# Performance work log

Hardware: AMD Instinct MI355X
Metric: run time of the kernel (lower is better)

The kernel has to match this reference:

```python
import jax, jax.numpy as jnp
import numpy as np

D = 1024       # hidden_size
H = 16         # num_heads
DH = D // H    # d_keys = d_values = 64
FF = int(D * 2.0)  # mlp hidden
EPS = 1e-6


def _ln(t):
    # LayerNorm, elementwise_affine=False
    mu = jnp.mean(t, axis=-1, keepdims=True)
    var = jnp.mean((t - mu) ** 2, axis=-1, keepdims=True)
    return (t - mu) * jax.lax.rsqrt(var + EPS)


def setup_inputs() -> dict:
    key = jax.random.key(0)
    ks = jax.random.split(key, 16)
    B, L = 2, 2048
    s = 0.02
    return {
        "x": jax.random.normal(ks[0], (B, L, D), jnp.float32),
        "c": jax.random.normal(ks[1], (B, 1, D), jnp.float32),
        "Wq": jax.random.normal(ks[2], (D, D), jnp.float32) * s,
        "bq": jnp.zeros((D,), jnp.float32),
        "Wk": jax.random.normal(ks[3], (D, D), jnp.float32) * s,
        "bk": jnp.zeros((D,), jnp.float32),
        "Wv": jax.random.normal(ks[4], (D, D), jnp.float32) * s,
        "bv": jnp.zeros((D,), jnp.float32),
        "Wo": jax.random.normal(ks[5], (D, D), jnp.float32) * s,
        "bo": jnp.zeros((D,), jnp.float32),
        "W1": jax.random.normal(ks[6], (D, FF), jnp.float32) * s,
        "b1": jnp.zeros((FF,), jnp.float32),
        "W2": jax.random.normal(ks[7], (FF, D), jnp.float32) * s,
        "b2": jnp.zeros((D,), jnp.float32),
        "Wada": jax.random.normal(ks[8], (D, 6 * D), jnp.float32) * s,
        "bada": jnp.zeros((6 * D,), jnp.float32),
    }


def reference(x, c, Wq, bq, Wk, bk, Wv, bv, Wo, bo, W1, b1, W2, b2, Wada, bada):
    B, L, _ = x.shape
    # adaLN-Zero modulation params (dropout layers act as identity in eval)
    ada = jax.nn.silu(c) @ Wada + bada  # [B,1,6D]
    shift_msa, scale_msa, gate_msa, shift_mlp, scale_mlp, gate_mlp = jnp.split(ada, 6, axis=-1)

    # --- attention branch ---
    h = _ln(x) * (1.0 + scale_msa) + shift_msa
    q = (h @ Wq + bq).reshape(B, L, H, DH)
    k = (h @ Wk + bk).reshape(B, L, H, DH)
    v = (h @ Wv + bv).reshape(B, L, H, DH)
    scale = 1.0 / np.sqrt(DH).astype(np.float32)
    scores = jnp.einsum('blhe,bshe->bhls', q, k)  # full LxL scores, as in source
    A = jax.nn.softmax(scale * scores, axis=-1)
    out = jnp.einsum('bhls,bshd->blhd', A, v)     # [B,L,H,DH]
    # mix=True: transpose(2,1) then view(B,L,-1) -> head/position mixing reshape
    out = jnp.transpose(out, (0, 2, 1, 3)).reshape(B, L, H * DH)
    x = x + gate_msa * (out @ Wo + bo)

    # --- MLP branch (exact GELU: nn.GELU() passed as act_layer) ---
    h2 = _ln(x) * (1.0 + scale_mlp) + shift_mlp
    m = jax.nn.gelu(h2 @ W1 + b1, approximate=False) @ W2 + b2
    return x + gate_mlp * m
```

## Files before the change

kernel.cpp:

```cpp
#include <hip/hip_runtime.h>
#include <hip/hip_bf16.h>

typedef unsigned short ushort_t;
typedef __bf16 bf16x8 __attribute__((ext_vector_type(8)));
typedef float f32x4 __attribute__((ext_vector_type(4)));

typedef unsigned int u32;
typedef u32 __attribute__((address_space(1))) global_u32;
typedef u32 __attribute__((address_space(3))) lds_u32;

#define D_ 1024
#define L_ 2048
#define B_ 2
#define H_ 16
#define DH_ 64
#define FF_ 2048
#define ADA_ 6144
#define BHL_ (B_ * H_ * L_)
#define PSTR 136

#define MFMA __builtin_amdgcn_mfma_f32_16x16x32_bf16

__device__ __forceinline__ ushort_t f2bf(float f) {
    union { float f; u32 u; } v; v.f = f;
    u32 r = v.u + 0x7fffu + ((v.u >> 16) & 1u);
    return (ushort_t)(r >> 16);
}

__device__ __forceinline__ void llds16(const ushort_t* src, ushort_t* dst) {
    __builtin_amdgcn_global_load_lds((global_u32*)src, (lds_u32*)dst, 16, 0, 0);
}

__global__ void transpose_w(const float* __restrict__ W, ushort_t* __restrict__ Wt,
                            int K, int N) {
    __shared__ float tile[64][65];
    int n0 = blockIdx.x * 64, k0 = blockIdx.y * 64;
    int t = threadIdx.x;
    for (int p = 0; p < 4; ++p) {
        int k = p * 16 + (t >> 4), nn = (t & 15) * 4;
        float4 v = *(const float4*)(W + (size_t)(k0 + k) * N + n0 + nn);
        tile[k][nn] = v.x; tile[k][nn + 1] = v.y; tile[k][nn + 2] = v.z; tile[k][nn + 3] = v.w;
    }
    __syncthreads();
    for (int p = 0; p < 4; ++p) {
        int n = p * 16 + (t >> 4), kk = (t & 15) * 4;
        ushort4 o;
        o.x = f2bf(tile[kk][n]); o.y = f2bf(tile[kk + 1][n]);
        o.z = f2bf(tile[kk + 2][n]); o.w = f2bf(tile[kk + 3][n]);
        *(ushort4*)(Wt + (size_t)(n0 + n) * K + k0 + kk) = o;
    }
}

__global__ void transpose_v(const ushort_t* __restrict__ V, ushort_t* __restrict__ Vt) {
    __shared__ ushort_t tile[64][72];
    int bh = blockIdx.y, l0 = blockIdx.x * 64;
    const ushort_t* Vb = V + ((size_t)bh * L_ + l0) * DH_;
    ushort_t* Vtb = Vt + (size_t)bh * DH_ * L_;
    int t = threadIdx.x;
    for (int p = 0; p < 2; ++p) {
        int i = p * 32 + (t >> 3), d0 = (t & 7) * 8;
        ushort4 v0 = *(const ushort4*)(Vb + (size_t)i * DH_ + d0);
        ushort4 v1 = *(const ushort4*)(Vb + (size_t)i * DH_ + d0 + 4);
        tile[d0 + 0][i] = v0.x; tile[d0 + 1][i] = v0.y; tile[d0 + 2][i] = v0.z; tile[d0 + 3][i] = v0.w;
        tile[d0 + 4][i] = v1.x; tile[d0 + 5][i] = v1.y; tile[d0 + 6][i] = v1.z; tile[d0 + 7][i] = v1.w;
    }
    __syncthreads();
    for (int p = 0; p < 2; ++p) {
        int dh = p * 32 + (t >> 3), j0 = (t & 7) * 8;
        ushort4 o0, o1;
        o0.x = tile[dh][j0 + 0]; o0.y = tile[dh][j0 + 1]; o0.z = tile[dh][j0 + 2]; o0.w = tile[dh][j0 + 3];
        o1.x = tile[dh][j0 + 4]; o1.y = tile[dh][j0 + 5]; o1.z = tile[dh][j0 + 6]; o1.w = tile[dh][j0 + 7];
        *(ushort4*)(Vtb + (size_t)dh * L_ + l0 + j0) = o0;
        *(ushort4*)(Vtb + (size_t)dh * L_ + l0 + j0 + 4) = o1;
    }
}

__global__ void ada_gemv(const float* __restrict__ c, const float* __restrict__ Wada,
                         float* __restrict__ partial) {
    int ks = blockIdx.y;
    int j = blockIdx.x * 256 + threadIdx.x;
    __shared__ float s0[64], s1[64];
    if (threadIdx.x < 64) {
        float v = c[ks * 64 + threadIdx.x];
        s0[threadIdx.x] = v / (1.f + __expf(-v));
        v = c[D_ + ks * 64 + threadIdx.x];
        s1[threadIdx.x] = v / (1.f + __expf(-v));
    }
    __syncthreads();
    float a0 = 0.f, a1 = 0.f;
#pragma unroll 8
    for (int d = 0; d < 64; ++d) {
        float w = Wada[(size_t)(ks * 64 + d) * ADA_ + j];
        a0 = fmaf(s0[d], w, a0);
        a1 = fmaf(s1[d], w, a1);
    }
    partial[(size_t)(ks * 2 + 0) * ADA_ + j] = a0;
    partial[(size_t)(ks * 2 + 1) * ADA_ + j] = a1;
}

__global__ void ada_reduce(const float* __restrict__ partial,
                           const float* __restrict__ bada, float* __restrict__ ada) {
    int j = blockIdx.x * 256 + threadIdx.x;
    float a0 = bada[j], a1 = bada[j];
#pragma unroll
    for (int ks = 0; ks < 16; ++ks) {
        a0 += partial[(size_t)(ks * 2 + 0) * ADA_ + j];
        a1 += partial[(size_t)(ks * 2 + 1) * ADA_ + j];
    }
    ada[j] = a0;
    ada[ADA_ + j] = a1;
}

__global__ void ln_mod(const float* __restrict__ x, const float* __restrict__ ada,
                       int so, int co, ushort_t* __restrict__ out) {
    int row = blockIdx.x;
    int b = row >> 11;
    float4 v = ((const float4*)(x + (size_t)row * D_))[threadIdx.x];
    float sum = v.x + v.y + v.z + v.w;
    float sq = v.x * v.x + v.y * v.y + v.z * v.z + v.w * v.w;
    for (int off = 32; off; off >>= 1) { sum += __shfl_down(sum, off); sq += __shfl_down(sq, off); }
    __shared__ float sa[4], sb[4];
    int wave = threadIdx.x >> 6, lane = threadIdx.x & 63;
    if (lane == 0) { sa[wave] = sum; sb[wave] = sq; }
    __syncthreads();
    sum = sa[0] + sa[1] + sa[2] + sa[3];
    sq = sb[0] + sb[1] + sb[2] + sb[3];
    float mean = sum * (1.f / 1024.f);
    float var = sq * (1.f / 1024.f) - mean * mean;
    float rstd = rsqrtf(var + 1e-6f);
    int d = threadIdx.x * 4;
    const float* shf = ada + (size_t)b * ADA_ + so;
    const float* scf = ada + (size_t)b * ADA_ + co;
    ushort4 ov;
    ov.x = f2bf((v.x - mean) * rstd * (1.f + scf[d + 0]) + shf[d + 0]);
    ov.y = f2bf((v.y - mean) * rstd * (1.f + scf[d + 1]) + shf[d + 1]);
    ov.z = f2bf((v.z - mean) * rstd * (1.f + scf[d + 2]) + shf[d + 2]);
    ov.w = f2bf((v.w - mean) * rstd * (1.f + scf[d + 3]) + shf[d + 3]);
    *(ushort4*)(out + (size_t)row * D_ + d) = ov;
}

struct EpiArgs {
    const float* bias0; const float* bias1; const float* bias2;
    ushort_t* o0; ushort_t* o1; ushort_t* o2;
    const float* resid; const float* gate;
    float* fout;
};

template <int EPI>
__device__ __forceinline__ void epi_store(float v, int m, int n, int N, const EpiArgs& e) {
    if (EPI == 0) {
        int which = n >> 10, cc = n & 1023;
        const float* bias = which == 0 ? e.bias0 : which == 1 ? e.bias1 : e.bias2;
        ushort_t* ob = which == 0 ? e.o0 : which == 1 ? e.o1 : e.o2;
        v += bias[cc];
        if (which == 0) v *= 0.18033688f;
        int b = m >> 11, l = m & 2047, h = cc >> 6, dh = cc & 63;
        ob[(((size_t)(b * H_ + h) * L_) + l) * DH_ + dh] = f2bf(v);
    } else if (EPI == 1) {
        v += e.bias0[n];
        v = 0.5f * v * (1.f + erff(v * 0.70710678118f));
        e.o0[(size_t)m * N + n] = f2bf(v);
    } else {
        int b = m >> 11;
        e.fout[(size_t)m * N + n] =
            e.resid[(size_t)m * N + n] + e.gate[(size_t)b * ADA_ + n] * (v + e.bias0[n]);
    }
}

template <int EPI>
__device__ __forceinline__ void st4(const f32x4& cc, int mb, int n, int N, const EpiArgs& e) {
#pragma unroll
    for (int r = 0; r < 4; ++r) epi_store<EPI>(cc[r], mb + r, n, N, e);
}

template <int EPI>
__global__ __launch_bounds__(256, 2) void gemm_bt(
    const ushort_t* __restrict__ A, const ushort_t* __restrict__ Bt,
    int M, int N, int K, EpiArgs e) {
    __shared__ ushort_t As[128 * 64];
    __shared__ ushort_t Bs[128 * 64];
    int m0 = blockIdx.x * 128, n0 = blockIdx.y * 128;
    int tid = threadIdx.x, wave = tid >> 6, lane = tid & 63;
    int quad = lane >> 4, lc = lane & 15;
    int wm = (wave & 1) * 64, wn = (wave >> 1) * 64;
    int srow = lane >> 3, sg = lane & 7;
    int sw = lc & 7;

    f32x4 c00 = {}, c01 = {}, c02 = {}, c03 = {};
    f32x4 c10 = {}, c11 = {}, c12 = {}, c13 = {};
    f32x4 c20 = {}, c21 = {}, c22 = {}, c23 = {};
    f32x4 c30 = {}, c31 = {}, c32 = {}, c33 = {};

    for (int k0 = 0; k0 < K; k0 += 64) {
#pragma unroll
        for (int i = 0; i < 8; ++i) {
            int chunk = wave * 8 + i;
            int c = chunk & 15;
            int row = c * 8 + srow;
            int g = sg ^ (row & 7);
            if (chunk < 16)
                llds16(A + (size_t)(m0 + row) * K + k0 + g * 8, &As[c * 512 + lane * 8]);
            else
                llds16(Bt + (size_t)(n0 + row) * K + k0 + g * 8, &Bs[c * 512 + lane * 8]);
        }
        __syncthreads();
#pragma unroll
        for (int kk = 0; kk < 2; ++kk) {
            int off = ((kk * 4 + quad) ^ sw) * 8;
            bf16x8 a0 = *(const bf16x8*)&As[(wm +  0 + lc) * 64 + off];
            bf16x8 a1 = *(const bf16x8*)&As[(wm + 16 + lc) * 64 + off];
            bf16x8 a2 = *(const bf16x8*)&As[(wm + 32 + lc) * 64 + off];
            bf16x8 a3 = *(const bf16x8*)&As[(wm + 48 + lc) * 64 + off];
            bf16x8 b0 = *(const bf16x8*)&Bs[(wn +  0 + lc) * 64 + off];
            bf16x8 b1 = *(const bf16x8*)&Bs[(wn + 16 + lc) * 64 + off];
            bf16x8 b2 = *(const bf16x8*)&Bs[(wn + 32 + lc) * 64 + off];
            bf16x8 b3 = *(const bf16x8*)&Bs[(wn + 48 + lc) * 64 + off];
            c00 = MFMA(a0, b0, c00, 0, 0, 0); c01 = MFMA(a0, b1, c01, 0, 0, 0);
            c02 = MFMA(a0, b2, c02, 0, 0, 0); c03 = MFMA(a0, b3, c03, 0, 0, 0);
            c10 = MFMA(a1, b0, c10, 0, 0, 0); c11 = MFMA(a1, b1, c11, 0, 0, 0);
            c12 = MFMA(a1, b2, c12, 0, 0, 0); c13 = MFMA(a1, b3, c13, 0, 0, 0);
            c20 = MFMA(a2, b0, c20, 0, 0, 0); c21 = MFMA(a2, b1, c21, 0, 0, 0);
            c22 = MFMA(a2, b2, c22, 0, 0, 0); c23 = MFMA(a2, b3, c23, 0, 0, 0);
            c30 = MFMA(a3, b0, c30, 0, 0, 0); c31 = MFMA(a3, b1, c31, 0, 0, 0);
            c32 = MFMA(a3, b2, c32, 0, 0, 0); c33 = MFMA(a3, b3, c33, 0, 0, 0);
        }
        __syncthreads();
    }

    int mb = m0 + wm + quad * 4, nb = n0 + wn + lc;
    st4<EPI>(c00, mb +  0, nb +  0, N, e); st4<EPI>(c01, mb +  0, nb + 16, N, e);
    st4<EPI>(c02, mb +  0, nb + 32, N, e); st4<EPI>(c03, mb +  0, nb + 48, N, e);
    st4<EPI>(c10, mb + 16, nb +  0, N, e); st4<EPI>(c11, mb + 16, nb + 16, N, e);
    st4<EPI>(c12, mb + 16, nb + 32, N, e); st4<EPI>(c13, mb + 16, nb + 48, N, e);
    st4<EPI>(c20, mb + 32, nb +  0, N, e); st4<EPI>(c21, mb + 32, nb + 16, N, e);
    st4<EPI>(c22, mb + 32, nb + 32, N, e); st4<EPI>(c23, mb + 32, nb + 48, N, e);
    st4<EPI>(c30, mb + 48, nb +  0, N, e); st4<EPI>(c31, mb + 48, nb + 16, N, e);
    st4<EPI>(c32, mb + 48, nb + 32, N, e); st4<EPI>(c33, mb + 48, nb + 48, N, e);
}

__global__ __launch_bounds__(256, 2) void attn(
    const ushort_t* __restrict__ Q, const ushort_t* __restrict__ Kx,
    const ushort_t* __restrict__ Vt,
    ushort_t* __restrict__ Op0, ushort_t* __restrict__ Op1,
    float* __restrict__ lsum) {
    __shared__ ushort_t Ks[128 * 64];
    __shared__ ushort_t Vs[64 * 128];
    __shared__ ushort_t Ps[4 * 16 * PSTR];
    int id = blockIdx.x;
    int bh = ((id & 7) << 2) + ((id >> 3) & 3);
    int half = (id >> 5) & 1;
    int qt = id >> 6;
    const ushort_t* Qg = Q + ((size_t)bh * L_ + qt * 128) * DH_;
    const ushort_t* Kg = Kx + (size_t)bh * L_ * DH_;
    const ushort_t* Vg = Vt + (size_t)bh * DH_ * L_;
    int tid = threadIdx.x, wave = tid >> 6, lane = tid & 63;
    int quad = lane >> 4, lc = lane & 15;
    int sw = lc & 7;
    int srow = lane >> 3, sg = lane & 7;

    const ushort_t* qp = Qg + (size_t)(wave * 32 + lc) * DH_ + quad * 8;
    bf16x8 q00 = *(const bf16x8*)(qp);
    bf16x8 q01 = *(const bf16x8*)(qp + 32);
    bf16x8 q10 = *(const bf16x8*)(qp + 16 * DH_);
    bf16x8 q11 = *(const bf16x8*)(qp + 16 * DH_ + 32);

    f32x4 o00 = {}, o01 = {}, o02 = {}, o03 = {};
    f32x4 o10 = {}, o11 = {}, o12 = {}, o13 = {};
    float lrow0 = 0.f, lrow1 = 0.f;
    ushort_t* Pw = &Ps[wave * 16 * PSTR];

    for (int t = half * 8; t < half * 8 + 8; ++t) {
#pragma unroll
        for (int i = 0; i < 8; ++i) {
            int chunk = wave * 8 + i;
            if (chunk < 16) {
                int row = chunk * 8 + srow;
                int g = sg ^ (row & 7);
                llds16(Kg + ((size_t)(t * 128 + row)) * DH_ + g * 8, &Ks[chunk * 512 + lane * 8]);
            } else {
                int c2 = chunk - 16;
                int row = c2 * 4 + (lane >> 4);
                int g = (lane & 15) ^ (row & 15);
                llds16(Vg + (size_t)row * L_ + t * 128 + g * 8, &Vs[c2 * 512 + lane * 8]);
            }
        }
        __syncthreads();

        f32x4 s[2][8];
#pragma unroll
        for (int kk = 0; kk < 2; ++kk) {
            int off = ((kk * 4 + quad) ^ sw) * 8;
            bf16x8 aq0 = kk == 0 ? q00 : q01;
            bf16x8 aq1 = kk == 0 ? q10 : q11;
#pragma unroll
            for (int ni = 0; ni < 8; ++ni) {
                bf16x8 bk = *(const bf16x8*)&Ks[(ni * 16 + lc) * 64 + off];
                if (kk == 0) {
                    f32x4 z = {0.f, 0.f, 0.f, 0.f};
                    s[0][ni] = MFMA(bk, aq0, z, 0, 0, 0);
                    s[1][ni] = MFMA(bk, aq1, z, 0, 0, 0);
                } else {
                    s[0][ni] = MFMA(bk, aq0, s[0][ni], 0, 0, 0);
                    s[1][ni] = MFMA(bk, aq1, s[1][ni], 0, 0, 0);
                }
            }
        }

#pragma unroll
        for (int pi = 0; pi < 2; ++pi) {
            float acc = 0.f;
#pragma unroll
            for (int ni = 0; ni < 8; ++ni) {
                float p0 = __builtin_amdgcn_exp2f(s[pi][ni][0]);
                float p1 = __builtin_amdgcn_exp2f(s[pi][ni][1]);
                float p2 = __builtin_amdgcn_exp2f(s[pi][ni][2]);
                float p3 = __builtin_amdgcn_exp2f(s[pi][ni][3]);
                acc += (p0 + p1) + (p2 + p3);
                u32 lo = (u32)f2bf(p0) | ((u32)f2bf(p1) << 16);
                u32 hi = (u32)f2bf(p2) | ((u32)f2bf(p3) << 16);
                uint2 pk; pk.x = lo; pk.y = hi;
                *(uint2*)&Pw[lc * PSTR + ni * 16 + quad * 4] = pk;
            }
            acc += __shfl_xor(acc, 16);
            acc += __shfl_xor(acc, 32);
            if (pi == 0) lrow0 += acc; else lrow1 += acc;

#pragma unroll
            for (int kk = 0; kk < 4; ++kk) {
                int gq = kk * 4 + quad;
                bf16x8 ap  = *(const bf16x8*)&Pw[lc * PSTR + gq * 8];
                bf16x8 bv0 = *(const bf16x8*)&Vs[( 0 + lc) * 128 + ((gq ^ lc) * 8)];
                bf16x8 bv1 = *(const bf16x8*)&Vs[(16 + lc) * 128 + ((gq ^ lc) * 8)];
                bf16x8 bv2 = *(const bf16x8*)&Vs[(32 + lc) * 128 + ((gq ^ lc) * 8)];
                bf16x8 bv3 = *(const bf16x8*)&Vs[(48 + lc) * 128 + ((gq ^ lc) * 8)];
                if (pi == 0) {
                    o00 = MFMA(ap, bv0, o00, 0, 0, 0); o01 = MFMA(ap, bv1, o01, 0, 0, 0);
                    o02 = MFMA(ap, bv2, o02, 0, 0, 0); o03 = MFMA(ap, bv3, o03, 0, 0, 0);
                } else {
                    o10 = MFMA(ap, bv0, o10, 0, 0, 0); o11 = MFMA(ap, bv1, o11, 0, 0, 0);
                    o12 = MFMA(ap, bv2, o12, 0, 0, 0); o13 = MFMA(ap, bv3, o13, 0, 0, 0);
                }
            }
        }
        __syncthreads();
    }

    ushort_t* Op = half ? Op1 : Op0;
#pragma unroll
    for (int pi = 0; pi < 2; ++pi) {
#pragma unroll
        for (int nio = 0; nio < 4; ++nio) {
            const f32x4& ov = pi == 0 ? (nio == 0 ? o00 : nio == 1 ? o01 : nio == 2 ? o02 : o03)
                                      : (nio == 0 ? o10 : nio == 1 ? o11 : nio == 2 ? o12 : o13);
#pragma unroll
            for (int r = 0; r < 4; ++r) {
                int row = qt * 128 + wave * 32 + pi * 16 + quad * 4 + r;
                Op[((size_t)bh * L_ + row) * DH_ + nio * 16 + lc] = f2bf(ov[r]);
            }
        }
    }
    if (quad == 0) {
        int base = qt * 128 + wave * 32;
        lsum[(size_t)half * BHL_ + (size_t)bh * L_ + base + lc] = lrow0;
        lsum[(size_t)half * BHL_ + (size_t)bh * L_ + base + 16 + lc] = lrow1;
    }
}

__global__ void attn_merge(const ushort_t* __restrict__ Op0,
                           const ushort_t* __restrict__ Op1,
                           const float* __restrict__ lsum,
                           ushort_t* __restrict__ O) {
    int gid = blockIdx.x * 256 + threadIdx.x;
    int row = gid >> 3, j = gid & 7;
    float inv = 1.f / (lsum[row] + lsum[BHL_ + row]);
    bf16x8 v0 = *(const bf16x8*)(Op0 + (size_t)row * DH_ + j * 8);
    bf16x8 v1 = *(const bf16x8*)(Op1 + (size_t)row * DH_ + j * 8);
    ushort4 lo, hi;
    lo.x = f2bf(((float)v0[0] + (float)v1[0]) * inv);
    lo.y = f2bf(((float)v0[1] + (float)v1[1]) * inv);
    lo.z = f2bf(((float)v0[2] + (float)v1[2]) * inv);
    lo.w = f2bf(((float)v0[3] + (float)v1[3]) * inv);
    hi.x = f2bf(((float)v0[4] + (float)v1[4]) * inv);
    hi.y = f2bf(((float)v0[5] + (float)v1[5]) * inv);
    hi.z = f2bf(((float)v0[6] + (float)v1[6]) * inv);
    hi.w = f2bf(((float)v0[7] + (float)v1[7]) * inv);
    *(ushort4*)(O + (size_t)row * DH_ + j * 8) = lo;
    *(ushort4*)(O + (size_t)row * DH_ + j * 8 + 4) = hi;
}

extern "C" void kernel_launch(void* const* d_in, const int* in_sizes, int n_in,
                              void* d_out, int out_size, void* d_ws, size_t ws_size,
                              hipStream_t stream) {
    (void)in_sizes; (void)n_in; (void)out_size; (void)ws_size;
    const float* x    = (const float*)d_in[0];
    const float* c    = (const float*)d_in[1];
    const float* Wq   = (const float*)d_in[2];
    const float* bq   = (const float*)d_in[3];
    const float* Wk   = (const float*)d_in[4];
    const float* bk   = (const float*)d_in[5];
    const float* Wv   = (const float*)d_in[6];
    const float* bv   = (const float*)d_in[7];
    const float* Wo   = (const float*)d_in[8];
    const float* bo   = (const float*)d_in[9];
    const float* W1   = (const float*)d_in[10];
    const float* b1   = (const float*)d_in[11];
    const float* W2   = (const float*)d_in[12];
    const float* b2   = (const float*)d_in[13];
    const float* Wada = (const float*)d_in[14];
    const float* bada = (const float*)d_in[15];

    char* w = (char*)d_ws;
    float*    ada  = (float*)(w + 0);
    ushort_t* Wqkv = (ushort_t*)(w + 49152);
    ushort_t* Wo_t = (ushort_t*)(w + 6340608);
    ushort_t* W1_t = (ushort_t*)(w + 8437760);
    ushort_t* W2_t = (ushort_t*)(w + 12632064);
    ushort_t* h    = (ushort_t*)(w + 16826368);
    ushort_t* Qb   = (ushort_t*)(w + 25214976);
    ushort_t* Kb   = (ushort_t*)(w + 33603584);
    ushort_t* Vb   = (ushort_t*)(w + 41992192);
    ushort_t* Vtb  = (ushort_t*)(w + 50380800);
    float*    x1   = (float*)(w + 58769408);
    ushort_t* Ob   = Qb;
    ushort_t* m1   = Qb;
    float*    lsb  = x1;
    float*    adap = (float*)Vtb;

    const int M = B_ * L_;

    transpose_w<<<dim3(16, 16), 256, 0, stream>>>(Wq, Wqkv + 0,             D_, D_);
    transpose_w<<<dim3(16, 16), 256, 0, stream>>>(Wk, Wqkv + 1024 * 1024,   D_, D_);
    transpose_w<<<dim3(16, 16), 256, 0, stream>>>(Wv, Wqkv + 2 * 1024 * 1024, D_, D_);
    transpose_w<<<dim3(16, 16), 256, 0, stream>>>(Wo, Wo_t, D_, D_);
    transpose_w<<<dim3(32, 16), 256, 0, stream>>>(W1, W1_t, D_, FF_);
    transpose_w<<<dim3(16, 32), 256, 0, stream>>>(W2, W2_t, FF_, D_);

    ada_gemv<<<dim3(24, 16), 256, 0, stream>>>(c, Wada, adap);
    ada_reduce<<<24, 256, 0, stream>>>(adap, bada, ada);
    ln_mod<<<M, 256, 0, stream>>>(x, ada, 0, 1024, h);

    EpiArgs e0 = {bq, bk, bv, Qb, Kb, Vb, nullptr, nullptr, nullptr};
    gemm_bt<0><<<dim3(32, 24), 256, 0, stream>>>(h, Wqkv, M, 3072, D_, e0);

    transpose_v<<<dim3(32, 32), 256, 0, stream>>>(Vb, Vtb);

    attn<<<1024, 256, 0, stream>>>(Qb, Kb, Vtb, Vb, h, lsb);
    attn_merge<<<2048, 256, 0, stream>>>(Vb, h, lsb, Ob);

    EpiArgs e1 = {bo, nullptr, nullptr, nullptr, nullptr, nullptr, x, ada + 2048, x1};
    gemm_bt<2><<<dim3(32, 8), 256, 0, stream>>>(Ob, Wo_t, M, D_, D_, e1);

    ln_mod<<<M, 256, 0, stream>>>(x1, ada, 3072, 4096, h);

    EpiArgs e2 = {b1, nullptr, nullptr, m1, nullptr, nullptr, nullptr, nullptr, nullptr};
    gemm_bt<1><<<dim3(32, 16), 256, 0, stream>>>(h, W1_t, M, FF_, D_, e2);

    EpiArgs e3 = {b2, nullptr, nullptr, nullptr, nullptr, nullptr, x1, ada + 5120, (float*)d_out};
    gemm_bt<2><<<dim3(32, 8), 256, 0, stream>>>(m1, W2_t, M, D_, FF_, e3);
}
```

Measured before the change: 370.8 us.

## Merge weight transposes, add 64-row GEMM for small grids, swizzle P tile

Folds the six weight-transpose launches into one 2048-block kernel to cut launch overhead. Adds a gemm_bt64 variant with 64x128 tiles and uses it for the Wo, W1 and W2 GEMMs, doubling the block count so the grid fills more of the GPU's compute units (a 256-block grid is smaller than the device). Replaces the padded P buffer in attention with an XOR-swizzled 128-wide layout to save LDS while avoiding bank conflicts. The smaller tiles lower per-block data reuse and raise total global and LDS traffic.

Measured after the change: 341.2 us. 1.09x faster.

```diff
diff --git a/kernel.cpp b/kernel.cpp
--- a/kernel.cpp
+++ b/kernel.cpp
@@ -17,7 +17,6 @@
 #define FF_ 2048
 #define ADA_ 6144
 #define BHL_ (B_ * H_ * L_)
-#define PSTR 136
 
 #define MFMA __builtin_amdgcn_mfma_f32_16x16x32_bf16
 
@@ -31,10 +30,25 @@
     __builtin_amdgcn_global_load_lds((global_u32*)src, (lds_u32*)dst, 16, 0, 0);
 }
 
-__global__ void transpose_w(const float* __restrict__ W, ushort_t* __restrict__ Wt,
-                            int K, int N) {
+__global__ void transpose_w_all(
+    const float* __restrict__ Wq, const float* __restrict__ Wk,
+    const float* __restrict__ Wv, const float* __restrict__ Wo,
+    const float* __restrict__ W1, const float* __restrict__ W2,
+    ushort_t* __restrict__ Wqkv, ushort_t* __restrict__ Wo_t,
+    ushort_t* __restrict__ W1_t, ushort_t* __restrict__ W2_t) {
     __shared__ float tile[64][65];
-    int n0 = blockIdx.x * 64, k0 = blockIdx.y * 64;
+    int id = blockIdx.x;
+    const float* W; ushort_t* Wt; int K, N, ntx, lid;
+    if (id < 1024) {
+        int which = id >> 8; lid = id & 255; K = 1024; N = 1024; ntx = 16;
+        W  = which == 0 ? Wq : which == 1 ? Wk : which == 2 ? Wv : Wo;
+        Wt = which == 3 ? Wo_t : Wqkv + (size_t)which * 1024 * 1024;
+    } else if (id < 1536) {
+        lid = id - 1024; W = W1; Wt = W1_t; K = 1024; N = 2048; ntx = 32;
+    } else {
+        lid = id - 1536; W = W2; Wt = W2_t; K = 2048; N = 1024; ntx = 16;
+    }
+    int n0 = (lid % ntx) * 64, k0 = (lid / ntx) * 64;
     int t = threadIdx.x;
     for (int p = 0; p < 4; ++p) {
         int k = p * 16 + (t >> 4), nn = (t & 15) * 4;
@@ -238,6 +252,64 @@
     st4<EPI>(c32, mb + 48, nb + 32, N, e); st4<EPI>(c33, mb + 48, nb + 48, N, e);
 }
 
+template <int EPI>
+__global__ __launch_bounds__(256, 2) void gemm_bt64(
+    const ushort_t* __restrict__ A, const ushort_t* __restrict__ Bt,
+    int M, int N, int K, EpiArgs e) {
+    __shared__ ushort_t As[64 * 64];
+    __shared__ ushort_t Bs[128 * 64];
+    int m0 = blockIdx.x * 64, n0 = blockIdx.y * 128;
+    int tid = threadIdx.x, wave = tid >> 6, lane = tid & 63;
+    int quad = lane >> 4, lc = lane & 15;
+    int wn = wave * 32;
+    int srow = lane >> 3, sg = lane & 7;
+    int sw = lc & 7;
+
+    f32x4 c00 = {}, c01 = {};
+    f32x4 c10 = {}, c11 = {};
+    f32x4 c20 = {}, c21 = {};
+    f32x4 c30 = {}, c31 = {};
+
+    for (int k0 = 0; k0 < K; k0 += 64) {
+#pragma unroll
+        for (int i = 0; i < 6; ++i) {
+            int chunk = wave * 6 + i;
+            if (chunk < 8) {
+                int row = chunk * 8 + srow;
+                int g = sg ^ (row & 7);
+                llds16(A + (size_t)(m0 + row) * K + k0 + g * 8, &As[chunk * 512 + lane * 8]);
+            } else {
+                int c = chunk - 8;
+                int row = c * 8 + srow;
+                int g = sg ^ (row & 7);
+                llds16(Bt + (size_t)(n0 + row) * K + k0 + g * 8, &Bs[c * 512 + lane * 8]);
+            }
+        }
+        __syncthreads();
+#pragma unroll
+        for (int kk = 0; kk < 2; ++kk) {
+            int off = ((kk * 4 + quad) ^ sw) * 8;
+            bf16x8 a0 = *(const bf16x8*)&As[( 0 + lc) * 64 + off];
+            bf16x8 a1 = *(const bf16x8*)&As[(16 + lc) * 64 + off];
+            bf16x8 a2 = *(const bf16x8*)&As[(32 + lc) * 64 + off];
+            bf16x8 a3 = *(const bf16x8*)&As[(48 + lc) * 64 + off];
+            bf16x8 b0 = *(const bf16x8*)&Bs[(wn +  0 + lc) * 64 + off];
+            bf16x8 b1 = *(const bf16x8*)&Bs[(wn + 16 + lc) * 64 + off];
+            c00 = MFMA(a0, b0, c00, 0, 0, 0); c01 = MFMA(a0, b1, c01, 0, 0, 0);
+            c10 = MFMA(a1, b0, c10, 0, 0, 0); c11 = MFMA(a1, b1, c11, 0, 0, 0);
+            c20 = MFMA(a2, b0, c20, 0, 0, 0); c21 = MFMA(a2, b1, c21, 0, 0, 0);
+            c30 = MFMA(a3, b0, c30, 0, 0, 0); c31 = MFMA(a3, b1, c31, 0, 0, 0);
+        }
+        __syncthreads();
+    }
+
+    int mb = m0 + quad * 4, nb = n0 + wn + lc;
+    st4<EPI>(c00, mb +  0, nb + 0, N, e); st4<EPI>(c01, mb +  0, nb + 16, N, e);
+    st4<EPI>(c10, mb + 16, nb + 0, N, e); st4<EPI>(c11, mb + 16, nb + 16, N, e);
+    st4<EPI>(c20, mb + 32, nb + 0, N, e); st4<EPI>(c21, mb + 32, nb + 16, N, e);
+    st4<EPI>(c30, mb + 48, nb + 0, N, e); st4<EPI>(c31, mb + 48, nb + 16, N, e);
+}
+
 __global__ __launch_bounds__(256, 2) void attn(
     const ushort_t* __restrict__ Q, const ushort_t* __restrict__ Kx,
     const ushort_t* __restrict__ Vt,
@@ -245,7 +317,7 @@
     float* __restrict__ lsum) {
     __shared__ ushort_t Ks[128 * 64];
     __shared__ ushort_t Vs[64 * 128];
-    __shared__ ushort_t Ps[4 * 16 * PSTR];
+    __shared__ ushort_t Ps[4 * 16 * 128];
     int id = blockIdx.x;
     int bh = ((id & 7) << 2) + ((id >> 3) & 3);
     int half = (id >> 5) & 1;
@@ -267,7 +339,7 @@
     f32x4 o00 = {}, o01 = {}, o02 = {}, o03 = {};
     f32x4 o10 = {}, o11 = {}, o12 = {}, o13 = {};
     float lrow0 = 0.f, lrow1 = 0.f;
-    ushort_t* Pw = &Ps[wave * 16 * PSTR];
+    ushort_t* Pw = &Ps[wave * 16 * 128];
 
     for (int t = half * 8; t < half * 8 + 8; ++t) {
 #pragma unroll
@@ -319,7 +391,8 @@
                 u32 lo = (u32)f2bf(p0) | ((u32)f2bf(p1) << 16);
                 u32 hi = (u32)f2bf(p2) | ((u32)f2bf(p3) << 16);
                 uint2 pk; pk.x = lo; pk.y = hi;
-                *(uint2*)&Pw[lc * PSTR + ni * 16 + quad * 4] = pk;
+                int cg = ni * 2 + (quad >> 1);
+                *(uint2*)&Pw[lc * 128 + ((cg ^ lc) & 15) * 8 + (quad & 1) * 4] = pk;
             }
             acc += __shfl_xor(acc, 16);
             acc += __shfl_xor(acc, 32);
@@ -328,7 +401,7 @@
 #pragma unroll
             for (int kk = 0; kk < 4; ++kk) {
                 int gq = kk * 4 + quad;
-                bf16x8 ap  = *(const bf16x8*)&Pw[lc * PSTR + gq * 8];
+                bf16x8 ap  = *(const bf16x8*)&Pw[lc * 128 + ((gq ^ lc) & 15) * 8];
                 bf16x8 bv0 = *(const bf16x8*)&Vs[( 0 + lc) * 128 + ((gq ^ lc) * 8)];
                 bf16x8 bv1 = *(const bf16x8*)&Vs[(16 + lc) * 128 + ((gq ^ lc) * 8)];
                 bf16x8 bv2 = *(const bf16x8*)&Vs[(32 + lc) * 128 + ((gq ^ lc) * 8)];
@@ -428,12 +501,8 @@
 
     const int M = B_ * L_;
 
-    transpose_w<<<dim3(16, 16), 256, 0, stream>>>(Wq, Wqkv + 0,             D_, D_);
-    transpose_w<<<dim3(16, 16), 256, 0, stream>>>(Wk, Wqkv + 1024 * 1024,   D_, D_);
-    transpose_w<<<dim3(16, 16), 256, 0, stream>>>(Wv, Wqkv + 2 * 1024 * 1024, D_, D_);
-    transpose_w<<<dim3(16, 16), 256, 0, stream>>>(Wo, Wo_t, D_, D_);
-    transpose_w<<<dim3(32, 16), 256, 0, stream>>>(W1, W1_t, D_, FF_);
-    transpose_w<<<dim3(16, 32), 256, 0, stream>>>(W2, W2_t, FF_, D_);
+    transpose_w_all<<<2048, 256, 0, stream>>>(Wq, Wk, Wv, Wo, W1, W2,
+                                              Wqkv, Wo_t, W1_t, W2_t);
 
     ada_gemv<<<dim3(24, 16), 256, 0, stream>>>(c, Wada, adap);
     ada_reduce<<<24, 256, 0, stream>>>(adap, bada, ada);
@@ -448,13 +517,13 @@
     attn_merge<<<2048, 256, 0, stream>>>(Vb, h, lsb, Ob);
 
     EpiArgs e1 = {bo, nullptr, nullptr, nullptr, nullptr, nullptr, x, ada + 2048, x1};
-    gemm_bt<2><<<dim3(32, 8), 256, 0, stream>>>(Ob, Wo_t, M, D_, D_, e1);
+    gemm_bt64<2><<<dim3(64, 8), 256, 0, stream>>>(Ob, Wo_t, M, D_, D_, e1);
 
     ln_mod<<<M, 256, 0, stream>>>(x1, ada, 3072, 4096, h);
 
     EpiArgs e2 = {b1, nullptr, nullptr, m1, nullptr, nullptr, nullptr, nullptr, nullptr};
-    gemm_bt<1><<<dim3(32, 16), 256, 0, stream>>>(h, W1_t, M, FF_, D_, e2);
+    gemm_bt64<1><<<dim3(64, 16), 256, 0, stream>>>(h, W1_t, M, FF_, D_, e2);
 
     EpiArgs e3 = {b2, nullptr, nullptr, nullptr, nullptr, nullptr, x1, ada + 5120, (float*)d_out};
-    gemm_bt<2><<<dim3(32, 8), 256, 0, stream>>>(m1, W2_t, M, D_, FF_, e3);
-}
+    gemm_bt64<2><<<dim3(64, 8), 256, 0, stream>>>(m1, W2_t, M, D_, FF_, e3);
+}
```
